# Performance work log

Hardware: AMD Instinct MI355X
Metric: run time of the kernel (lower is better)

The kernel has to match this reference:

```python
import jax, jax.numpy as jnp
import numpy as np

NUM_HEADS = 12

def setup_inputs() -> dict:
    key = jax.random.key(0)
    k1, k2, k3, k4 = jax.random.split(key, 4)
    B, N, D = 8, 1024, 768
    x = jax.random.normal(k1, (B, N, D), dtype=jnp.float32)
    mask = jax.random.randint(k2, (B, N), 0, 2, dtype=jnp.int32)
    Wqkv = jax.random.normal(k3, (3 * D, D), dtype=jnp.float32) * (D ** -0.5)
    Wproj = jax.random.normal(k4, (D, D), dtype=jnp.float32) * (D ** -0.5)
    bproj = jnp.zeros((D,), dtype=jnp.float32)
    return {"x": x, "mask": mask, "Wqkv": Wqkv, "Wproj": Wproj, "bproj": bproj}

def reference(x, mask, Wqkv, Wproj, bproj):
    B, N, D = x.shape
    H = NUM_HEADS
    hd = D // H
    scale = hd ** -0.5
    # QKV projection (no bias), split into q,k,v of shape [B,H,N,hd]
    qkv = jnp.einsum('bnd,ed->bne', x, Wqkv).reshape(B, N, 3, H, hd)
    qkv = jnp.transpose(qkv, (2, 0, 3, 1, 4))
    q, k, v = qkv[0], qkv[1], qkv[2]
    # padding mask: attend where both query and key are valid; masked-out
    # (padded) query rows attend only to themselves (diagonal) to avoid NaNs
    m = mask.astype(bool)  # [B,N]
    pair = m[:, None, :, None] & m[:, None, None, :]          # [B,1,N,N]
    diag = jnp.eye(N, dtype=bool)[None, None]                 # [1,1,N,N]
    attn_mask = pair | (diag & ~m[:, None, :, None])          # [B,1,N,N]
    scores = jnp.einsum('bhnd,bhmd->bhnm', q, k) * scale      # [B,H,N,N]
    scores = jnp.where(attn_mask, scores, jnp.finfo(scores.dtype).min)
    attn = jax.nn.softmax(scores, axis=-1)
    out = jnp.einsum('bhnm,bhmd->bhnd', attn, v)
    out = jnp.transpose(out, (0, 2, 1, 3)).reshape(B, N, D)
    out = jnp.einsum('bnd,ed->bne', out, Wproj) + bproj
    return out
```

## Files before the change

kernel.cpp:

```cpp
#include <hip/hip_runtime.h>
#include <hip/hip_bf16.h>
#include <stdint.h>


typedef unsigned short u16;
typedef __attribute__((ext_vector_type(8))) short short8;
typedef __attribute__((ext_vector_type(4))) float f32x4;

#define MFMA16(a, b, c) __builtin_amdgcn_mfma_f32_16x16x32_bf16((a), (b), (c), 0, 0, 0)

static __device__ __forceinline__ u16 f2bf(float f) {
    __hip_bfloat16 h = __float2bfloat16(f);
    return *(u16*)&h;
}
static __device__ __forceinline__ void gld16(const u16* g, u16* l) {
  __builtin_amdgcn_global_load_lds(
      (const __attribute__((address_space(1))) void*)g,
      (__attribute__((address_space(3))) void*)l, 16, 0, 0);
}

__global__ __launch_bounds__(256) void cvt_bf16(
    const float* __restrict__ s0, u16* __restrict__ d0, int n0,
    const float* __restrict__ s1, u16* __restrict__ d1, int n1,
    const float* __restrict__ s2, u16* __restrict__ d2, int n2) {
  int i = (blockIdx.x * 256 + threadIdx.x) * 4;
  const float* s; u16* d;
  if (i < n0) { s = s0 + i; d = d0 + i; }
  else if ((i -= n0) < n1) { s = s1 + i; d = d1 + i; }
  else if ((i -= n1) < n2) { s = s2 + i; d = d2 + i; }
  else return;
  float4 v = *(const float4*)s;
  ushort4 o;
  o.x = f2bf(v.x); o.y = f2bf(v.y); o.z = f2bf(v.z); o.w = f2bf(v.w);
  *(ushort4*)d = o;
}

__global__ __launch_bounds__(512, 4) void gemm_qkv_p32(
    const u16* __restrict__ A,
    const u16* __restrict__ B,
    u16* __restrict__ C) {
  constexpr int K = 768, LDC = 2304, NTIL = K / 32;
  __shared__ u16 lds[2][(256 + 128) * 32];
  const int tid = threadIdx.x;
  const int w = tid >> 6, l = tid & 63;
  const int lane16 = l & 15, quad = l >> 4;
  const int wr = w >> 2, wc = w & 3;

  const int orig = blockIdx.x;
  const int logical = (orig & 7) * 72 + (orig >> 3);
  const int i0 = (logical / 18) * 256, j0 = (logical % 18) * 128;

  f32x4 acc[8][2];
  #pragma unroll
  for (int m = 0; m < 8; m++)
    #pragma unroll
    for (int n = 0; n < 2; n++) acc[m][n] = (f32x4){0.f, 0.f, 0.f, 0.f};

  auto stage = [&](int buf, int t) {
    const int k0 = t * 32;
    u16* Ad = &lds[buf][0];
    #pragma unroll
    for (int s = 0; s < 2; s++) {
      int lin = tid + s * 512;
      int row = lin >> 2, j = lin & 3;
      gld16(&A[(size_t)(i0 + row) * K + k0 + ((j ^ ((row >> 1) & 3)) * 8)], &Ad[lin * 8]);
    }
    {
      u16* Bd = &lds[buf][256 * 32];
      int row = tid >> 2, j = tid & 3;
      gld16(&B[(size_t)(j0 + row) * K + k0 + ((j ^ ((row >> 1) & 3)) * 8)], &Bd[tid * 8]);
    }
  };

  stage(0, 0);
  stage(1, 1);
  asm volatile("s_waitcnt vmcnt(3)" ::: "memory");
  __builtin_amdgcn_s_barrier();

  for (int t = 0; t < NTIL; t++) {
    const u16* Al = &lds[t & 1][0];
    const u16* Bl = &lds[t & 1][256 * 32];
    short8 bf[2];
    #pragma unroll
    for (int n = 0; n < 2; n++) {
      int row = wc * 32 + n * 16 + lane16;
      int ch = quad ^ ((row >> 1) & 3);
      bf[n] = *(const short8*)&Bl[row * 32 + ch * 8];
    }
    #pragma unroll
    for (int p = 0; p < 2; p++) {
      short8 af[4];
      #pragma unroll
      for (int mi = 0; mi < 4; mi++) {
        int row = wr * 128 + (4 * p + mi) * 16 + lane16;
        int ch = quad ^ ((row >> 1) & 3);
        af[mi] = *(const short8*)&Al[row * 32 + ch * 8];
      }
      if (p == 1) {
        asm volatile("s_waitcnt lgkmcnt(0)" ::: "memory");
        __builtin_amdgcn_sched_barrier(0);
        __builtin_amdgcn_s_barrier();
        if (t + 2 < NTIL) stage(t & 1, t + 2);
      }
      __builtin_amdgcn_s_setprio(1);
      #pragma unroll
      for (int mi = 0; mi < 4; mi++)
        #pragma unroll
        for (int n = 0; n < 2; n++)
          acc[4 * p + mi][n] = MFMA16(af[mi], bf[n], acc[4 * p + mi][n]);
      __builtin_amdgcn_s_setprio(0);
    }
    if (t + 2 < NTIL) asm volatile("s_waitcnt vmcnt(3)" ::: "memory");
    else              asm volatile("s_waitcnt vmcnt(0)" ::: "memory");
    __builtin_amdgcn_s_barrier();
  }

  #pragma unroll
  for (int m = 0; m < 8; m++) {
    #pragma unroll
    for (int n = 0; n < 2; n++) {
      int col = j0 + wc * 32 + n * 16 + lane16;
      #pragma unroll
      for (int r = 0; r < 4; r++) {
        int row = i0 + wr * 128 + m * 16 + quad * 4 + r;
        C[(size_t)row * LDC + col] = f2bf(acc[m][n][r]);
      }
    }
  }
}

template<int K, int BN, int LDC, bool BF16OUT, int NXB>
__global__ __launch_bounds__(256) void gemm_bt(
    const u16* __restrict__ A,
    const u16* __restrict__ B,
    void* __restrict__ Cout,
    const float* __restrict__ bias) {
  constexpr int NT = BN / 32;
  __shared__ u16 As[128 * 32];
  __shared__ u16 Bs[BN * 32];
  const int tid = threadIdx.x;
  const int w = tid >> 6, l = tid & 63;
  const int lane16 = l & 15, quad = l >> 4;

  constexpr int nwg = NXB * 64;
  constexpr int qch = nwg / 8;
  const int orig = blockIdx.x;
  const int logical = (orig & 7) * qch + (orig >> 3);
  const int i0 = (logical / NXB) * 128, j0 = (logical % NXB) * BN;

  const int mh = (w & 1) * 64;
  const int nh = (w >> 1) * (BN / 2);

  f32x4 acc[4][NT];
  #pragma unroll
  for (int mt = 0; mt < 4; mt++)
    #pragma unroll
    for (int nt = 0; nt < NT; nt++) acc[mt][nt] = (f32x4){0.f, 0.f, 0.f, 0.f};

  for (int kt = 0; kt < K / 32; kt++) {
    const int k0 = kt * 32;
    __syncthreads();
    #pragma unroll
    for (int s = 0; s < 2; s++) {
      int idx = tid + s * 256;
      int row = idx >> 2, c8 = (idx & 3) * 8;
      gld16(&A[(size_t)(i0 + row) * K + k0 + c8], &As[idx * 8]);
    }
    #pragma unroll
    for (int s = 0; s < BN / 64; s++) {
      int idx = tid + s * 256;
      int row = idx >> 2, c8 = (idx & 3) * 8;
      gld16(&B[(size_t)(j0 + row) * K + k0 + c8], &Bs[idx * 8]);
    }
    __syncthreads();

    short8 af[4], bf[NT];
    #pragma unroll
    for (int mt = 0; mt < 4; mt++)
      af[mt] = *(const short8*)&As[(mh + mt * 16 + lane16) * 32 + quad * 8];
    #pragma unroll
    for (int nt = 0; nt < NT; nt++)
      bf[nt] = *(const short8*)&Bs[(nh + nt * 16 + lane16) * 32 + quad * 8];
    #pragma unroll
    for (int mt = 0; mt < 4; mt++)
      #pragma unroll
      for (int nt = 0; nt < NT; nt++)
        acc[mt][nt] = MFMA16(af[mt], bf[nt], acc[mt][nt]);
  }

  #pragma unroll
  for (int mt = 0; mt < 4; mt++) {
    #pragma unroll
    for (int nt = 0; nt < NT; nt++) {
      int col = j0 + nh + nt * 16 + lane16;
      #pragma unroll
      for (int r = 0; r < 4; r++) {
        int row = i0 + mh + mt * 16 + quad * 4 + r;
        if (BF16OUT) {
          ((u16*)Cout)[(size_t)row * LDC + col] = f2bf(acc[mt][nt][r]);
        } else {
          ((float*)Cout)[(size_t)row * LDC + col] = acc[mt][nt][r] + bias[col];
        }
      }
    }
  }
}

__global__ __launch_bounds__(256, 3) void attn_mfma(
    const u16* __restrict__ qkv,
    const int* __restrict__ mask,
    u16* __restrict__ ctx) {
  __shared__ u16 Ks[64][72];
  __shared__ u16 Vt[64][72];
  __shared__ u16 Ps[4][32][72];
  __shared__ float mkb_all[1024];

  const int tid = threadIdx.x;
  const int w = tid >> 6, l = tid & 63;
  const int lane16 = l & 15, quad = l >> 4;
  const int idx = blockIdx.x;
  const int bh = idx % 96;
  const int rb = idx / 96;
  const int b = bh / 12, h = bh % 12;
  const int n0 = rb * 128;
  const int baseRow = b * 1024;

  const float K1 = 0.18033688011112043f;
  const float K0 = -23.083120654223415f;

  const int key_s = tid >> 2, ds_s = (tid & 3) * 16;
  const int kA_s = (tid & 31) * 2, dg_s = tid >> 5;

  {
    int4 mv = *(const int4*)&mask[baseRow + tid * 4];
    f32x4 mf;
    mf[0] = mv.x ? K0 : -1e38f;
    mf[1] = mv.y ? K0 : -1e38f;
    mf[2] = mv.z ? K0 : -1e38f;
    mf[3] = mv.w ? K0 : -1e38f;
    *(f32x4*)&mkb_all[tid * 4] = mf;
  }

  short8 qfrag[2][2];
  #pragma unroll
  for (int qt = 0; qt < 2; qt++) {
    const u16* qp = qkv + (size_t)(baseRow + n0 + w*32 + qt*16 + lane16) * 2304 + h*64;
    #pragma unroll
    for (int ks = 0; ks < 2; ks++)
      qfrag[qt][ks] = *(const short8*)(qp + ks*32 + quad*8);
  }

  f32x4 oacc[2][4];
  #pragma unroll
  for (int qt = 0; qt < 2; qt++)
    #pragma unroll
    for (int nt = 0; nt < 4; nt++) oacc[qt][nt] = (f32x4){0.f, 0.f, 0.f, 0.f};
  f32x4 lsum4[2] = {(f32x4){0.f,0.f,0.f,0.f}, (f32x4){0.f,0.f,0.f,0.f}};

  uint4 kr0, kr1, vr0, vr1;
  {
    const u16* kp = qkv + (size_t)(baseRow + key_s) * 2304 + 768 + h*64 + ds_s;
    kr0 = *(const uint4*)kp;
    kr1 = *(const uint4*)(kp + 8);
    const u16* vp = qkv + (size_t)(baseRow + kA_s) * 2304 + 1536 + h*64 + dg_s*8;
    vr0 = *(const uint4*)vp;
    vr1 = *(const uint4*)(vp + 2304);
  }

  for (int c = 0; c < 16; c++) {
    if (c) __syncthreads();

    *(uint4*)&Ks[key_s][ds_s]     = kr0;
    *(uint4*)&Ks[key_s][ds_s + 8] = kr1;
    {
      const u16* va = (const u16*)&vr0;
      const u16* vb = (const u16*)&vr1;
      #pragma unroll
      for (int j = 0; j < 8; j++)
        *(unsigned int*)&Vt[dg_s*8 + j][kA_s] =
            (unsigned int)va[j] | ((unsigned int)vb[j] << 16);
    }

    if (c + 1 < 16) {
      const u16* kp = qkv + (size_t)(baseRow + (c+1)*64 + key_s) * 2304 + 768 + h*64 + ds_s;
      kr0 = *(const uint4*)kp;
      kr1 = *(const uint4*)(kp + 8);
      const u16* vp = qkv + (size_t)(baseRow + (c+1)*64 + kA_s) * 2304 + 1536 + h*64 + dg_s*8;
      vr0 = *(const uint4*)vp;
      vr1 = *(const uint4*)(vp + 2304);
    }
    __syncthreads();

    f32x4 sacc[4][2];
    #pragma unroll
    for (int kt = 0; kt < 4; kt++)
      #pragma unroll
      for (int qt = 0; qt < 2; qt++) sacc[kt][qt] = (f32x4){0.f, 0.f, 0.f, 0.f};
    #pragma unroll
    for (int ks = 0; ks < 2; ks++) {
      short8 kf[4];
      #pragma unroll
      for (int kt = 0; kt < 4; kt++)
        kf[kt] = *(const short8*)&Ks[kt*16 + lane16][ks*32 + quad*8];
      __builtin_amdgcn_s_setprio(1);
      #pragma unroll
      for (int kt = 0; kt < 4; kt++)
        #pragma unroll
        for (int qt = 0; qt < 2; qt++)
          sacc[kt][qt] = MFMA16(kf[kt], qfrag[qt][ks], sacc[kt][qt]);
      __builtin_amdgcn_s_setprio(0);
    }

    #pragma unroll
    for (int kt = 0; kt < 4; kt++) {
      f32x4 mk4 = *(const f32x4*)&mkb_all[c*64 + kt*16 + quad*4];
      #pragma unroll
      for (int qt = 0; qt < 2; qt++) {
        float e0 = __builtin_amdgcn_exp2f(fmaf(sacc[kt][qt][0], K1, mk4[0]));
        float e1 = __builtin_amdgcn_exp2f(fmaf(sacc[kt][qt][1], K1, mk4[1]));
        float e2 = __builtin_amdgcn_exp2f(fmaf(sacc[kt][qt][2], K1, mk4[2]));
        float e3 = __builtin_amdgcn_exp2f(fmaf(sacc[kt][qt][3], K1, mk4[3]));
        lsum4[qt][0] += e0; lsum4[qt][1] += e1;
        lsum4[qt][2] += e2; lsum4[qt][3] += e3;
        uint2 pv;
        asm("v_cvt_pk_bf16_f32 %0, %1, %2" : "=v"(pv.x) : "v"(e0), "v"(e1));
        asm("v_cvt_pk_bf16_f32 %0, %1, %2" : "=v"(pv.y) : "v"(e2), "v"(e3));
        *(uint2*)&Ps[w][qt*16 + lane16][kt*16 + quad*4] = pv;
      }
    }

    #pragma unroll
    for (int kc = 0; kc < 2; kc++) {
      short8 pf[2], vf[4];
      #pragma unroll
      for (int qt = 0; qt < 2; qt++)
        pf[qt] = *(const short8*)&Ps[w][qt*16 + lane16][kc*32 + quad*8];
      #pragma unroll
      for (int nt = 0; nt < 4; nt++)
        vf[nt] = *(const short8*)&Vt[nt*16 + lane16][kc*32 + quad*8];
      __builtin_amdgcn_s_setprio(1);
      #pragma unroll
      for (int qt = 0; qt < 2; qt++)
        #pragma unroll
        for (int nt = 0; nt < 4; nt++)
          oacc[qt][nt] = MFMA16(pf[qt], vf[nt], oacc[qt][nt]);
      __builtin_amdgcn_s_setprio(0);
    }
  }

  float linv[2][4];
  #pragma unroll
  for (int qt = 0; qt < 2; qt++) {
    float s = lsum4[qt][0] + lsum4[qt][1] + lsum4[qt][2] + lsum4[qt][3];
    s += __shfl_xor(s, 16);
    s += __shfl_xor(s, 32);
    #pragma unroll
    for (int r = 0; r < 4; r++)
      linv[qt][r] = 1.0f / __shfl(s, quad*4 + r);
  }
  #pragma unroll
  for (int qt = 0; qt < 2; qt++) {
    #pragma unroll
    for (int r = 0; r < 4; r++) {
      int rl = w*32 + qt*16 + quad*4 + r;
      int rg = n0 + rl;
      int mq = (mkb_all[n0 + rl] != -1e38f);
      #pragma unroll
      for (int nt = 0; nt < 4; nt++) {
        u16 outv;
        if (mq) {
          outv = f2bf(oacc[qt][nt][r] * linv[qt][r]);
        } else {
          outv = qkv[(size_t)(baseRow + rg) * 2304 + 1536 + h*64 + nt*16 + lane16];
        }
        ctx[(size_t)(baseRow + rg) * 768 + h*64 + nt*16 + lane16] = outv;
      }
    }
  }
}

extern "C" void kernel_launch(void* const* d_in, const int* in_sizes, int n_in,
                              void* d_out, int out_size, void* d_ws, size_t ws_size,
                              hipStream_t stream) {
  const float* x     = (const float*)d_in[0];
  const int*   mask  = (const int*)d_in[1];
  const float* Wqkv  = (const float*)d_in[2];
  const float* Wproj = (const float*)d_in[3];
  const float* bproj = (const float*)d_in[4];
  float* out = (float*)d_out;

  const int NX = 8192 * 768;
  const int NQ = 2304 * 768;
  const int NP = 768 * 768;

  char* wsb = (char*)d_ws;
  u16* qkv    = (u16*)wsb;
  u16* ctx    = (u16*)(wsb + (size_t)8192 * 2304 * 2);
  u16* xb     = (u16*)(wsb + (size_t)8192 * 2304 * 2 + (size_t)8192 * 768 * 2);
  u16* wqkvb  = xb + NX;
  u16* wprojb = wqkvb + NQ;

  int cvt_blocks = ((NX + NQ + NP) / 4 + 255) / 256;
  cvt_bf16<<<dim3(cvt_blocks), 256, 0, stream>>>(x, xb, NX, Wqkv, wqkvb, NQ, Wproj, wprojb, NP);

  gemm_qkv_p32<<<dim3(576), 512, 0, stream>>>(xb, wqkvb, qkv);
  attn_mfma<<<dim3(768), 256, 0, stream>>>(qkv, mask, ctx);
  gemm_bt<768, 64, 768, false, 12><<<dim3(12 * 64), 256, 0, stream>>>(ctx, wprojb, out, bproj);
}
```

Before: 186.0 us.

## Double-buffer output projection GEMM with swizzled LDS and async prefetch

Replaces the generic single-buffered projection GEMM with a dedicated kernel that double-buffers LDS tiles, prefetching the tile two steps ahead while MFMAs run on the current one. LDS chunk addresses are XOR-swizzled to reduce bank conflicts, and instruction priority is raised around the MFMA blocks. This is meant to hide global-load latency and remove a barrier per k-step. The cost is a larger LDS footprint and more delicate waitcnt/barrier sequencing.

```diff
diff --git a/kernel.cpp b/kernel.cpp
--- a/kernel.cpp
+++ b/kernel.cpp
@@ -4,6 +4,7 @@
 
 
 typedef unsigned short u16;
+typedef unsigned int u32;
 typedef __attribute__((ext_vector_type(8))) short short8;
 typedef __attribute__((ext_vector_type(4))) float f32x4;
 
@@ -129,78 +130,97 @@
   }
 }
 
-template<int K, int BN, int LDC, bool BF16OUT, int NXB>
-__global__ __launch_bounds__(256) void gemm_bt(
+__global__ __launch_bounds__(256, 3) void gemm_proj_p32(
     const u16* __restrict__ A,
     const u16* __restrict__ B,
-    void* __restrict__ Cout,
+    float* __restrict__ C,
     const float* __restrict__ bias) {
-  constexpr int NT = BN / 32;
-  __shared__ u16 As[128 * 32];
-  __shared__ u16 Bs[BN * 32];
+  constexpr int K = 768, LDC = 768, NTIL = K / 32;
+  __shared__ u16 lds[2][(128 + 64) * 32];
   const int tid = threadIdx.x;
   const int w = tid >> 6, l = tid & 63;
   const int lane16 = l & 15, quad = l >> 4;
-
-  constexpr int nwg = NXB * 64;
-  constexpr int qch = nwg / 8;
+  const int mh = (w & 1) * 64;
+  const int nh = (w >> 1) * 32;
+
   const int orig = blockIdx.x;
-  const int logical = (orig & 7) * qch + (orig >> 3);
-  const int i0 = (logical / NXB) * 128, j0 = (logical % NXB) * BN;
-
-  const int mh = (w & 1) * 64;
-  const int nh = (w >> 1) * (BN / 2);
-
-  f32x4 acc[4][NT];
-  #pragma unroll
-  for (int mt = 0; mt < 4; mt++)
-    #pragma unroll
-    for (int nt = 0; nt < NT; nt++) acc[mt][nt] = (f32x4){0.f, 0.f, 0.f, 0.f};
-
-  for (int kt = 0; kt < K / 32; kt++) {
-    const int k0 = kt * 32;
-    __syncthreads();
+  const int logical = (orig & 7) * 96 + (orig >> 3);
+  const int i0 = (logical / 12) * 128, j0 = (logical % 12) * 64;
+
+  f32x4 acc[4][2];
+  #pragma unroll
+  for (int m = 0; m < 4; m++)
+    #pragma unroll
+    for (int n = 0; n < 2; n++) acc[m][n] = (f32x4){0.f, 0.f, 0.f, 0.f};
+
+  auto stage = [&](int buf, int t) {
+    const int k0 = t * 32;
+    u16* Ad = &lds[buf][0];
     #pragma unroll
     for (int s = 0; s < 2; s++) {
-      int idx = tid + s * 256;
-      int row = idx >> 2, c8 = (idx & 3) * 8;
-      gld16(&A[(size_t)(i0 + row) * K + k0 + c8], &As[idx * 8]);
-    }
-    #pragma unroll
-    for (int s = 0; s < BN / 64; s++) {
-      int idx = tid + s * 256;
-      int row = idx >> 2, c8 = (idx & 3) * 8;
-      gld16(&B[(size_t)(j0 + row) * K + k0 + c8], &Bs[idx * 8]);
-    }
-    __syncthreads();
-
-    short8 af[4], bf[NT];
-    #pragma unroll
-    for (int mt = 0; mt < 4; mt++)
-      af[mt] = *(const short8*)&As[(mh + mt * 16 + lane16) * 32 + quad * 8];
-    #pragma unroll
-    for (int nt = 0; nt < NT; nt++)
-      bf[nt] = *(const short8*)&Bs[(nh + nt * 16 + lane16) * 32 + quad * 8];
-    #pragma unroll
-    for (int mt = 0; mt < 4; mt++)
-      #pragma unroll
-      for (int nt = 0; nt < NT; nt++)
-        acc[mt][nt] = MFMA16(af[mt], bf[nt], acc[mt][nt]);
-  }
-
-  #pragma unroll
-  for (int mt = 0; mt < 4; mt++) {
-    #pragma unroll
-    for (int nt = 0; nt < NT; nt++) {
-      int col = j0 + nh + nt * 16 + lane16;
+      int lin = tid + s * 256;
+      int row = lin >> 2, j = lin & 3;
+      gld16(&A[(size_t)(i0 + row) * K + k0 + ((j ^ ((row >> 1) & 3)) * 8)], &Ad[lin * 8]);
+    }
+    {
+      u16* Bd = &lds[buf][128 * 32];
+      int row = tid >> 2, j = tid & 3;
+      gld16(&B[(size_t)(j0 + row) * K + k0 + ((j ^ ((row >> 1) & 3)) * 8)], &Bd[tid * 8]);
+    }
+  };
+
+  stage(0, 0);
+  stage(1, 1);
+  asm volatile("s_waitcnt vmcnt(3)" ::: "memory");
+  __builtin_amdgcn_s_barrier();
+
+  for (int t = 0; t < NTIL; t++) {
+    const u16* Al = &lds[t & 1][0];
+    const u16* Bl = &lds[t & 1][128 * 32];
+    short8 bf[2];
+    #pragma unroll
+    for (int n = 0; n < 2; n++) {
+      int row = nh + n * 16 + lane16;
+      int ch = quad ^ ((row >> 1) & 3);
+      bf[n] = *(const short8*)&Bl[row * 32 + ch * 8];
+    }
+    #pragma unroll
+    for (int p = 0; p < 2; p++) {
+      short8 af[2];
+      #pragma unroll
+      for (int mi = 0; mi < 2; mi++) {
+        int row = mh + (2 * p + mi) * 16 + lane16;
+        int ch = quad ^ ((row >> 1) & 3);
+        af[mi] = *(const short8*)&Al[row * 32 + ch * 8];
+      }
+      if (p == 1) {
+        asm volatile("s_waitcnt lgkmcnt(0)" ::: "memory");
+        __builtin_amdgcn_sched_barrier(0);
+        __builtin_amdgcn_s_barrier();
+        if (t + 2 < NTIL) stage(t & 1, t + 2);
+      }
+      __builtin_amdgcn_s_setprio(1);
+      #pragma unroll
+      for (int mi = 0; mi < 2; mi++)
+        #pragma unroll
+        for (int n = 0; n < 2; n++)
+          acc[2 * p + mi][n] = MFMA16(af[mi], bf[n], acc[2 * p + mi][n]);
+      __builtin_amdgcn_s_setprio(0);
+    }
+    if (t + 2 < NTIL) asm volatile("s_waitcnt vmcnt(3)" ::: "memory");
+    else              asm volatile("s_waitcnt vmcnt(0)" ::: "memory");
+    __builtin_amdgcn_s_barrier();
+  }
+
+  #pragma unroll
+  for (int m = 0; m < 4; m++) {
+    #pragma unroll
+    for (int n = 0; n < 2; n++) {
+      int col = j0 + nh + n * 16 + lane16;
       #pragma unroll
       for (int r = 0; r < 4; r++) {
-        int row = i0 + mh + mt * 16 + quad * 4 + r;
-        if (BF16OUT) {
-          ((u16*)Cout)[(size_t)row * LDC + col] = f2bf(acc[mt][nt][r]);
-        } else {
-          ((float*)Cout)[(size_t)row * LDC + col] = acc[mt][nt][r] + bias[col];
-        }
+        int row = i0 + mh + m * 16 + quad * 4 + r;
+        C[(size_t)row * LDC + col] = acc[m][n][r] + bias[col];
       }
     }
   }
@@ -405,5 +425,5 @@
 
   gemm_qkv_p32<<<dim3(576), 512, 0, stream>>>(xb, wqkvb, qkv);
   attn_mfma<<<dim3(768), 256, 0, stream>>>(qkv, mask, ctx);
-  gemm_bt<768, 64, 768, false, 12><<<dim3(12 * 64), 256, 0, stream>>>(ctx, wprojb, out, bproj);
-}
+  gemm_proj_p32<<<dim3(768), 256, 0, stream>>>(ctx, wprojb, out, bproj);
+}
```

Result: no change. 184.2 us (-0.9%).
